# Optimization experiments

Hardware: AMD Instinct MI355X
Metric: run time of the kernel (lower is better)

## Reference

```python
import jax, jax.numpy as jnp
import numpy as np

CLASSES = 21
IOU_THRESH = 0.5
ALPHA = 0.25   # focal loss alpha
GAMMA = 2.0    # focal loss gamma
SL1_BETA = 1.0 # torch SmoothL1Loss default beta
CLS_W = 1.0
REG_W = 1.0
NUM_ANCHORS = 98304
NUM_TARGETS = 1024


def _compute_iou(boxes_a, boxes_b):
    # boxes_a: [T,4], boxes_b: [A,4] in (x1,y1,x2,y2) -> [T,A]
    lt = jnp.maximum(boxes_a[:, None, :2], boxes_b[None, :, :2])
    rb = jnp.minimum(boxes_a[:, None, 2:], boxes_b[None, :, 2:])
    wh = jnp.clip(rb - lt, 0.0)
    inter = wh[..., 0] * wh[..., 1]
    area_a = (boxes_a[:, 2] - boxes_a[:, 0]) * (boxes_a[:, 3] - boxes_a[:, 1])
    area_b = (boxes_b[:, 2] - boxes_b[:, 0]) * (boxes_b[:, 3] - boxes_b[:, 1])
    union = area_a[:, None] + area_b[None, :] - inter
    return inter / jnp.maximum(union, 1e-8)


def _encode(boxes, anchors):
    bw = boxes[:, 2] - boxes[:, 0]
    bh = boxes[:, 3] - boxes[:, 1]
    bcx = boxes[:, 0] + 0.5 * bw
    bcy = boxes[:, 1] + 0.5 * bh
    aw = anchors[:, 2] - anchors[:, 0]
    ah = anchors[:, 3] - anchors[:, 1]
    acx = anchors[:, 0] + 0.5 * aw
    acy = anchors[:, 1] + 0.5 * ah
    tx = (bcx - acx) / aw
    ty = (bcy - acy) / ah
    tw = jnp.log(jnp.maximum(bw, 1e-8) / aw)
    th = jnp.log(jnp.maximum(bh, 1e-8) / ah)
    return jnp.stack([tx, ty, tw, th], axis=1)


def _focal_loss(logits, targets):
    # elementwise sigmoid focal loss (no reduction)
    p = jax.nn.sigmoid(logits)
    # numerically stable BCE with logits
    ce = jnp.maximum(logits, 0.0) - logits * targets + jnp.log1p(jnp.exp(-jnp.abs(logits)))
    p_t = p * targets + (1.0 - p) * (1.0 - targets)
    alpha_t = ALPHA * targets + (1.0 - ALPHA) * (1.0 - targets)
    return alpha_t * (1.0 - p_t) ** GAMMA * ce


def _smooth_l1(diff):
    ad = jnp.abs(diff)
    return jnp.where(ad < SL1_BETA, 0.5 * diff * diff / SL1_BETA, ad - 0.5 * SL1_BETA)


def setup_inputs() -> dict:
    key = jax.random.key(0)
    kA, kW, kT, kJ, kL, kC, kB = jax.random.split(key, 7)
    A, T = NUM_ANCHORS, NUM_TARGETS
    centers = jax.random.uniform(kA, (A, 2), minval=0.15, maxval=0.85)
    sizes = jax.random.uniform(kW, (A, 2), minval=0.05, maxval=0.30)
    anchors = jnp.concatenate([centers - 0.5 * sizes, centers + 0.5 * sizes], axis=1)
    # targets = jittered anchors so IoU >= 0.5 matches exist
    idx = jax.random.randint(kT, (T,), 0, A)
    jitter = jax.random.uniform(kJ, (T, 4), minval=-0.01, maxval=0.01)
    target_boxes = anchors[idx] + jitter
    target_labels = jax.random.randint(kL, (T,), 0, CLASSES)
    classification_preds = jax.random.normal(kC, (A, CLASSES), dtype=jnp.float32)
    boxes_preds = jax.random.normal(kB, (A, 4), dtype=jnp.float32)
    return {
        'classification_preds': classification_preds,
        'boxes_preds': boxes_preds,
        'anchors': anchors,
        'target_boxes': target_boxes,
        'target_labels': target_labels,
    }


def reference(classification_preds, boxes_preds, anchors, target_boxes, target_labels):
    iou = _compute_iou(target_boxes, anchors)  # [T, A]

    # anchor-side matching -> classification targets
    max_iou_for_anchors = jnp.max(iou, axis=0)          # [A]
    target_ids_for_anchors = jnp.argmax(iou, axis=0)     # [A]
    positive_mask = max_iou_for_anchors >= IOU_THRESH    # [A] bool
    n_pos = jnp.sum(positive_mask.astype(jnp.float32))
    onehot = jax.nn.one_hot(target_labels[target_ids_for_anchors], CLASSES, dtype=jnp.float32)
    cls_targets = jnp.where(positive_mask[:, None], onehot, 0.0)
    cls_loss = jnp.sum(_focal_loss(classification_preds, cls_targets)) / n_pos

    max_iou_for_targets = jnp.max(iou, axis=1)          # [T]
    anchor_ids_for_targets = jnp.argmax(iou, axis=1)     # [T]
    t_mask = (max_iou_for_targets >= IOU_THRESH).astype(jnp.float32)  # [T]
    matched_anchors = anchors[anchor_ids_for_targets]    # [T,4]
    encoded = _encode(target_boxes, matched_anchors)     # [T,4]
    pred = boxes_preds[anchor_ids_for_targets]           # [T,4]
    diff = (pred - encoded) * t_mask[:, None]
    n_match = jnp.maximum(jnp.sum(t_mask), 1.0)
    reg_loss = jnp.sum(_smooth_l1(diff)) / (n_match * 4.0)  # mean over matched elements

    w_cls = cls_loss * CLS_W
    w_reg = reg_loss * REG_W
    return (w_cls + w_reg, w_cls, w_reg)
```

## Files before the change

kernel.cpp:

```cpp
#include <hip/hip_runtime.h>
#include <stdint.h>

#define NA 98304
#define NT 1024
#define NC 21
#define NBLK 1536
#define HI_MIN 0xBF000000u
#define C3S 0.33333f

typedef unsigned int u32;
typedef unsigned long long u64;


__device__ __forceinline__ float f0(float x) {
    const float ax = fabsf(x);
    const float u  = __expf(-ax);
    const float ce = fmaxf(x, 0.f) + __logf(1.f + u);
    const float p  = (x >= 0.f ? 1.f : u) / (1.f + u);
    return 0.75f * p * p * ce;
}
__device__ __forceinline__ float f1(float x) {
    const float ax = fabsf(x);
    const float u  = __expf(-ax);
    const float ce = fmaxf(x, 0.f) - x + __logf(1.f + u);
    const float p  = (x >= 0.f ? 1.f : u) / (1.f + u);
    const float q  = 1.f - p;
    return 0.25f * q * q * ce;
}
__device__ __forceinline__ u64 mk_key(float iou, u32 idx) {
    return ((u64)(__float_as_uint(iou) | 0x80000000u) << 32) |
           (u64)(0xFFFFFFFFu - idx);
}
__device__ __forceinline__ float smooth_l1(float d) {
    const float ad = fabsf(d);
    return (ad < 1.f) ? 0.5f * d * d : ad - 0.5f;
}
__device__ __forceinline__ u64 aload64(const u64* p) {
    return __hip_atomic_load(p, __ATOMIC_RELAXED, __HIP_MEMORY_SCOPE_AGENT);
}
__device__ __forceinline__ float aloadf(const float* p) {
    return __hip_atomic_load(p, __ATOMIC_RELAXED, __HIP_MEMORY_SCOPE_AGENT);
}
__device__ __forceinline__ int aloadi(const int* p) {
    return __hip_atomic_load(p, __ATOMIC_RELAXED, __HIP_MEMORY_SCOPE_AGENT);
}

#define CHECK(k, tkk)                                                       \
    {                                                                       \
        const float w0 = fminf(ac.z, tz[k]) + fminf(ac.x, ntx[k]);          \
        const float w  = fmaxf(w0, 0.f);                                    \
        const float h0 = fminf(ac.w, tw4[k]) + fminf(ac.y, nty[k]);         \
        if (fmaf(w, h0, narc) >= sac[k]) {                                  \
            const float h     = fmaxf(h0, 0.f);                             \
            const float inter = w * h;                                      \
            const float arj   = (ac.z + ac.x) * (ac.w + ac.y);              \
            const float sa    = (tz[k] + ntx[k]) * (tw4[k] + nty[k]);       \
            const float uni   = (arj + sa) - inter;                         \
            const float iou   = inter / uni;                                \
            const u64 nk = mk_key(iou, (u32)(b * 64 + j));                  \
            if (nk > tkk) tkk = nk;                                         \
            atomicMax(&s_ak[j], mk_key(iou, (u32)(t0 + 64 * k)));           \
        }                                                                   \
    }

__global__ __launch_bounds__(256) void k_all(
    const float* __restrict__ preds,
    const float4* __restrict__ preds4,
    const int* __restrict__ tlabels,
    const float4* __restrict__ anchors,
    const float4* __restrict__ tboxes,
    const float4* __restrict__ bpreds,
    u64* __restrict__ tkeys,
    float* __restrict__ part,
    int* __restrict__ npos_part,
    int* __restrict__ done_g,
    int* __restrict__ done2,
    float* __restrict__ out)
{
    __shared__ float4 s_anc[64];
    __shared__ float  s_narc[64];
    __shared__ u64    s_ak[64];
    __shared__ float  s_f[4];
    __shared__ int    s_fin;
    __shared__ double s_d[4];
    __shared__ int    s_i[4];
    __shared__ float  s_s[4], s_m[4];

    const int tid  = threadIdx.x;
    const int b    = blockIdx.x;
    const int lane = tid & 63, wid = tid >> 6;

    if (tid < 64) {
        const float4 A = anchors[b * 64 + tid];
        s_anc[tid]  = make_float4(-A.x, -A.y, A.z, A.w);
        s_narc[tid] = -(((A.z - A.x) * (A.w - A.y)) * C3S);
        s_ak[tid]   = 0ull;
    }

    const int t0 = wid * 256 + lane;
    float tz[4], ntx[4], tw4[4], nty[4], sac[4];
    #pragma unroll
    for (int k = 0; k < 4; ++k) {
        const float4 tb = tboxes[t0 + 64 * k];
        tz[k]  = tb.z;  ntx[k] = -tb.x;
        tw4[k] = tb.w;  nty[k] = -tb.y;
        sac[k] = ((tb.z - tb.x) * (tb.w - tb.y)) * C3S;
    }

    float facc;
    {
        const int pb = b * 336;
        const float4 v0 = preds4[pb + tid];
        facc = (f0(v0.x) + f0(v0.y)) + (f0(v0.z) + f0(v0.w));
        if (tid < 80) {
            const float4 v1 = preds4[pb + 256 + tid];
            facc += (f0(v1.x) + f0(v1.y)) + (f0(v1.z) + f0(v1.w));
        }
    }

    u64 tk0 = 0ull, tk1 = 0ull, tk2 = 0ull, tk3 = 0ull;
    __syncthreads();

    #pragma unroll 8
    for (int j = 0; j < 64; ++j) {
        const float4 ac  = s_anc[j];
        const float narc = s_narc[j];
        CHECK(0, tk0)
        CHECK(1, tk1)
        CHECK(2, tk2)
        CHECK(3, tk3)
    }

    for (int o = 32; o > 0; o >>= 1) facc += __shfl_down(facc, o);
    if (lane == 0) s_f[wid] = facc;

    if (tk0 != 0ull) atomicMax(&tkeys[t0],       tk0);
    if (tk1 != 0ull) atomicMax(&tkeys[t0 +  64], tk1);
    if (tk2 != 0ull) atomicMax(&tkeys[t0 + 128], tk2);
    if (tk3 != 0ull) atomicMax(&tkeys[t0 + 192], tk3);

    __syncthreads();

    float corrv = 0.f;
    int   cnt   = 0;
    if (tid < 64) {
        const u64 k0 = s_ak[tid];
        if ((u32)(k0 >> 32) >= HI_MIN) {
            cnt = 1;
            const int tI  = (int)(0xFFFFFFFFu - (u32)k0);
            const int lab = tlabels[tI];
            const float x = preds[(b * 64 + tid) * NC + lab];
            corrv = f1(x) - f0(x);
        }
        for (int o = 32; o > 0; o >>= 1) {
            corrv += __shfl_down(corrv, o);
            cnt   += __shfl_down(cnt, o);
        }
    }
    if (tid == 0) {
        __hip_atomic_store(&part[b], (s_f[0] + s_f[1] + s_f[2] + s_f[3]) + corrv,
                           __ATOMIC_RELAXED, __HIP_MEMORY_SCOPE_AGENT);
        __hip_atomic_store(&npos_part[b], cnt,
                           __ATOMIC_RELAXED, __HIP_MEMORY_SCOPE_AGENT);
    }
    __syncthreads();
    if (tid == 0) {
        __threadfence();
        int fin = 0;
        if (atomicAdd(&done_g[b & 63], 1) == 23) {
            __threadfence();
            fin = (atomicAdd(done2, 1) == 63);
        }
        s_fin = fin;
    }
    __syncthreads();
    if (!s_fin) return;
    __builtin_amdgcn_fence(__ATOMIC_ACQUIRE, "agent");

    double cl = 0.0;
    int    np = 0;
    #pragma unroll
    for (int j = 0; j < 6; ++j) {
        const int i = tid + 256 * j;
        cl += (double)aloadf(&part[i]);
        np += aloadi(&npos_part[i]);
    }
    float s = 0.f, m = 0.f;
    #pragma unroll
    for (int j = 0; j < 4; ++j) {
        const int t = tid + 256 * j;
        const u64 key = aload64(&tkeys[t]);
        if ((u32)(key >> 32) >= HI_MIN) {
            const u32 ga = 0xFFFFFFFFu - (u32)key;
            const float4 tb  = tboxes[t];
            const float4 abx = anchors[ga];
            const float4 pb  = bpreds[ga];
            const float bw = tb.z - tb.x, bh = tb.w - tb.y;
            const float bcx = tb.x + 0.5f * bw, bcy = tb.y + 0.5f * bh;
            const float aw = abx.z - abx.x, ah = abx.w - abx.y;
            const float acx = abx.x + 0.5f * aw, acy = abx.y + 0.5f * ah;
            const float tx = (bcx - acx) / aw;
            const float ty = (bcy - acy) / ah;
            const float tw = logf(fmaxf(bw, 1e-8f) / aw);
            const float th = logf(fmaxf(bh, 1e-8f) / ah);
            s += smooth_l1(pb.x - tx) + smooth_l1(pb.y - ty) +
                 smooth_l1(pb.z - tw) + smooth_l1(pb.w - th);
            m += 1.f;
        }
    }
    for (int o = 32; o > 0; o >>= 1) {
        cl += __shfl_down(cl, o);
        np += __shfl_down(np, o);
        s  += __shfl_down(s, o);
        m  += __shfl_down(m, o);
    }
    __syncthreads();
    if (lane == 0) { s_d[wid] = cl; s_i[wid] = np; s_s[wid] = s; s_m[wid] = m; }
    __syncthreads();
    if (tid == 0) {
        const double cls_sum = s_d[0] + s_d[1] + s_d[2] + s_d[3];
        const int    npos    = s_i[0] + s_i[1] + s_i[2] + s_i[3];
        const float  rs      = s_s[0] + s_s[1] + s_s[2] + s_s[3];
        const float  rm      = s_m[0] + s_m[1] + s_m[2] + s_m[3];
        const float cls = (float)(cls_sum / (double)npos);
        const float reg = rs / (fmaxf(rm, 1.f) * 4.f);
        out[0] = cls + reg;
        out[1] = cls;
        out[2] = reg;
    }
}

extern "C" void kernel_launch(void* const* d_in, const int* in_sizes, int n_in,
                              void* d_out, int out_size, void* d_ws, size_t ws_size,
                              hipStream_t stream) {
    const float*  preds   = (const float*)d_in[0];
    const float4* preds4  = (const float4*)d_in[0];
    const float4* bpreds  = (const float4*)d_in[1];
    const float4* anchors = (const float4*)d_in[2];
    const float4* tboxes  = (const float4*)d_in[3];
    const int*    tlabels = (const int*)d_in[4];

    char* ws = (char*)d_ws;
    int*  done2     = (int*)(ws + 0);
    int*  done_g    = (int*)(ws + 128);
    float* part     = (float*)(ws + 1024);
    int*  npos_part = (int*)(ws + 8192);
    u64*  tkeys     = (u64*)(ws + 16384);

    hipMemsetAsync(d_ws, 0, 1024, stream);

    k_all<<<dim3(NBLK), 256, 0, stream>>>(
        preds, preds4, tlabels, anchors, tboxes, bpreds,
        tkeys, part, npos_part, done_g, done2, (float*)d_out);
}
```

Measured before the change: 127.5 us.

## Bucket anchors spatially and cull targets per bucket before IoU matching

Adds a scatter kernel that bins anchors into 4096 buckets by center position and size, then each main block processes one bucket and keeps only the targets whose centers fall near the bucket's bounding range, so IoU is evaluated on far fewer anchor-target pairs than the dense 64x1024 tile. Overflowing anchors go to a spill list that the final block handles serially. The cost is an extra kernel launch, global atomics for bucketing, and a larger memset. The spill path is sequential with block-wide syncs per anchor and could be slow if many anchors spill.

New measurement: 192.2 us. 1.51x slower.

```diff
diff --git a/kernel.cpp b/kernel.cpp
--- a/kernel.cpp
+++ b/kernel.cpp
@@ -4,7 +4,9 @@
 #define NA 98304
 #define NT 1024
 #define NC 21
-#define NBLK 1536
+#define NBUCK 4096
+#define CAP 64
+#define GRID_MAIN 4096
 #define HI_MIN 0xBF000000u
 #define C3S 0.33333f
 
@@ -44,44 +46,93 @@
 __device__ __forceinline__ int aloadi(const int* p) {
     return __hip_atomic_load(p, __ATOMIC_RELAXED, __HIP_MEMORY_SCOPE_AGENT);
 }
-
-#define CHECK(k, tkk)                                                       \
+__device__ __forceinline__ int iclamp(int v, int lo, int hi) {
+    return v < lo ? lo : (v > hi ? hi : v);
+}
+
+__global__ __launch_bounds__(256) void k_scatter(
+    const float4* __restrict__ anchors,
+    float4* __restrict__ sortedA, u32* __restrict__ sortedId,
+    int* __restrict__ cursor, int* __restrict__ spillcnt,
+    float4* __restrict__ spillA, u32* __restrict__ spillId)
+{
+    const int a = blockIdx.x * 256 + threadIdx.x;
+    const float4 A = anchors[a];
+    const float acx = (A.x + A.z) * 0.5f, acy = (A.y + A.w) * 0.5f;
+    const float aw  = A.z - A.x,          ah  = A.w - A.y;
+    const int cx = iclamp((int)((acx - 0.15f) * 22.857143f), 0, 15);
+    const int cy = iclamp((int)((acy - 0.15f) * 22.857143f), 0, 15);
+    const int wc = iclamp((int)((aw - 0.05f) * 16.f), 0, 3);
+    const int hc = iclamp((int)((ah - 0.05f) * 16.f), 0, 3);
+    const int bkt = cx + (cy << 4) + ((wc + (hc << 2)) << 8);
+    const int pos = atomicAdd(&cursor[bkt], 1);
+    if (pos < CAP) {
+        sortedA[bkt * CAP + pos]  = A;
+        sortedId[bkt * CAP + pos] = (u32)a;
+    } else {
+        const int sp = atomicAdd(spillcnt, 1);
+        spillA[sp]  = A;
+        spillId[sp] = (u32)a;
+    }
+}
+
+#define SECTION(KKBASE)                                                     \
     {                                                                       \
-        const float w0 = fminf(ac.z, tz[k]) + fminf(ac.x, ntx[k]);          \
-        const float w  = fmaxf(w0, 0.f);                                    \
-        const float h0 = fminf(ac.w, tw4[k]) + fminf(ac.y, nty[k]);         \
-        if (fmaf(w, h0, narc) >= sac[k]) {                                  \
-            const float h     = fmaxf(h0, 0.f);                             \
-            const float inter = w * h;                                      \
-            const float arj   = (ac.z + ac.x) * (ac.w + ac.y);              \
-            const float sa    = (tz[k] + ntx[k]) * (tw4[k] + nty[k]);       \
-            const float uni   = (arj + sa) - inter;                         \
-            const float iou   = inter / uni;                                \
-            const u64 nk = mk_key(iou, (u32)(b * 64 + j));                  \
-            if (nk > tkk) tkk = nk;                                         \
-            atomicMax(&s_ak[j], mk_key(iou, (u32)(t0 + 64 * k)));           \
+        const int s  = tid + (KKBASE);                                      \
+        const bool vs = s < nf;                                             \
+        const float4 tb = vs ? s_ft[s] : make_float4(-1e30f,-1e30f,-1e30f,-1e30f); \
+        const float sacv = vs ? s_fs[s] : 1e30f;                            \
+        const int   fid  = vs ? s_fid[s] : 0;                               \
+        u64 tk = 0ull;                                                      \
+        _Pragma("unroll 2")                                                 \
+        for (int j = 0; j < cnt; ++j) {                                     \
+            const float4 ac  = s_anc[j];                                    \
+            const float narc = s_narc[j];                                   \
+            const float w0 = fminf(ac.z, tb.z) + fminf(ac.x, tb.x);         \
+            const float w  = fmaxf(w0, 0.f);                                \
+            const float h0 = fminf(ac.w, tb.w) + fminf(ac.y, tb.y);         \
+            if (fmaf(w, h0, narc) >= sacv) {                                \
+                const float h     = fmaxf(h0, 0.f);                         \
+                const float inter = w * h;                                  \
+                const float arj   = (ac.z + ac.x) * (ac.w + ac.y);          \
+                const float sa    = (tb.z + tb.x) * (tb.w + tb.y);          \
+                const float uni   = (arj + sa) - inter;                     \
+                const float iou   = inter / uni;                            \
+                const u64 nk = mk_key(iou, s_aid[j]);                       \
+                if (nk > tk) tk = nk;                                       \
+                atomicMax(&s_ak[j], mk_key(iou, (u32)fid));                 \
+            }                                                               \
         }                                                                   \
-    }
-
-__global__ __launch_bounds__(256) void k_all(
+        if (tk != 0ull) atomicMax(&tkeys[fid], tk);                         \
+    }
+
+__global__ __launch_bounds__(256) void k_main(
     const float* __restrict__ preds,
     const float4* __restrict__ preds4,
     const int* __restrict__ tlabels,
     const float4* __restrict__ anchors,
     const float4* __restrict__ tboxes,
     const float4* __restrict__ bpreds,
+    const float4* __restrict__ sortedA, const u32* __restrict__ sortedId,
+    const int* __restrict__ cursor, const int* __restrict__ spillcnt,
+    const float4* __restrict__ spillA, const u32* __restrict__ spillId,
     u64* __restrict__ tkeys,
-    float* __restrict__ part,
-    int* __restrict__ npos_part,
-    int* __restrict__ done_g,
-    int* __restrict__ done2,
+    float* __restrict__ part, int* __restrict__ npos_part,
+    int* __restrict__ done_g, int* __restrict__ done2,
     float* __restrict__ out)
 {
-    __shared__ float4 s_anc[64];
-    __shared__ float  s_narc[64];
-    __shared__ u64    s_ak[64];
+    __shared__ float4 s_anc[CAP];
+    __shared__ float  s_narc[CAP];
+    __shared__ u32    s_aid[CAP];
+    __shared__ u64    s_ak[CAP];
+    __shared__ float4 s_ft[NT];
+    __shared__ float  s_fs[NT];
+    __shared__ int    s_fid[NT];
+    __shared__ int    s_nf;
+    __shared__ float  s_bb[6];
     __shared__ float  s_f[4];
     __shared__ int    s_fin;
+    __shared__ u64    s_sp[4];
     __shared__ double s_d[4];
     __shared__ int    s_i[4];
     __shared__ float  s_s[4], s_m[4];
@@ -89,26 +140,11 @@
     const int tid  = threadIdx.x;
     const int b    = blockIdx.x;
     const int lane = tid & 63, wid = tid >> 6;
-
-    if (tid < 64) {
-        const float4 A = anchors[b * 64 + tid];
-        s_anc[tid]  = make_float4(-A.x, -A.y, A.z, A.w);
-        s_narc[tid] = -(((A.z - A.x) * (A.w - A.y)) * C3S);
-        s_ak[tid]   = 0ull;
-    }
-
-    const int t0 = wid * 256 + lane;
-    float tz[4], ntx[4], tw4[4], nty[4], sac[4];
-    #pragma unroll
-    for (int k = 0; k < 4; ++k) {
-        const float4 tb = tboxes[t0 + 64 * k];
-        tz[k]  = tb.z;  ntx[k] = -tb.x;
-        tw4[k] = tb.w;  nty[k] = -tb.y;
-        sac[k] = ((tb.z - tb.x) * (tb.w - tb.y)) * C3S;
-    }
-
-    float facc;
-    {
+    const int cnt0 = cursor[b];
+    const int cnt  = cnt0 > CAP ? CAP : cnt0;
+
+    float facc = 0.f;
+    if (b < 1536) {
         const int pb = b * 336;
         const float4 v0 = preds4[pb + tid];
         facc = (f0(v0.x) + f0(v0.y)) + (f0(v0.z) + f0(v0.w));
@@ -118,56 +154,96 @@
         }
     }
 
-    u64 tk0 = 0ull, tk1 = 0ull, tk2 = 0ull, tk3 = 0ull;
-    __syncthreads();
-
-    #pragma unroll 8
-    for (int j = 0; j < 64; ++j) {
-        const float4 ac  = s_anc[j];
-        const float narc = s_narc[j];
-        CHECK(0, tk0)
-        CHECK(1, tk1)
-        CHECK(2, tk2)
-        CHECK(3, tk3)
+    if (tid < CAP) {
+        const bool v = tid < cnt;
+        float4 A = make_float4(1e30f, 1e30f, -1e30f, -1e30f);
+        u32 id = 0u;
+        if (v) { A = sortedA[b * CAP + tid]; id = sortedId[b * CAP + tid]; }
+        s_anc[tid]  = make_float4(-A.x, -A.y, A.z, A.w);
+        s_narc[tid] = v ? -(((A.z - A.x) * (A.w - A.y)) * C3S) : -1e30f;
+        s_aid[tid]  = id;
+        s_ak[tid]   = 0ull;
+        const float cx = (A.x + A.z) * 0.5f, cy = (A.y + A.w) * 0.5f;
+        float c1 = v ? cx : 1e30f,  c2 = v ? cx : -1e30f;
+        float c3 = v ? cy : 1e30f,  c4 = v ? cy : -1e30f;
+        float c5 = v ? (A.z - A.x) : 0.f, c6 = v ? (A.w - A.y) : 0.f;
+        for (int o = 32; o > 0; o >>= 1) {
+            c1 = fminf(c1, __shfl_xor(c1, o));
+            c2 = fmaxf(c2, __shfl_xor(c2, o));
+            c3 = fminf(c3, __shfl_xor(c3, o));
+            c4 = fmaxf(c4, __shfl_xor(c4, o));
+            c5 = fmaxf(c5, __shfl_xor(c5, o));
+            c6 = fmaxf(c6, __shfl_xor(c6, o));
+        }
+        if (tid == 0) {
+            s_bb[0] = c1; s_bb[1] = c2; s_bb[2] = c3;
+            s_bb[3] = c4; s_bb[4] = c5; s_bb[5] = c6;
+            s_nf = 0;
+        }
+    }
+    __syncthreads();
+
+    if (cnt > 0) {
+        const float bxl = s_bb[0], bxh = s_bb[1], byl = s_bb[2], byh = s_bb[3];
+        const float awm = s_bb[4], ahm = s_bb[5];
+        #pragma unroll
+        for (int k = 0; k < 4; ++k) {
+            const int t = tid + 256 * k;
+            const float4 tb = tboxes[t];
+            const float tcx = (tb.x + tb.z) * 0.5f, tcy = (tb.y + tb.w) * 0.5f;
+            const float tw = tb.z - tb.x, th = tb.w - tb.y;
+            const float rx = (awm + tw) * 0.5f - fmaxf(awm, tw) * (1.f/3.f) + 1e-3f;
+            const float ry = (ahm + th) * 0.5f - fmaxf(ahm, th) * (1.f/3.f) + 1e-3f;
+            if (tcx >= bxl - rx && tcx <= bxh + rx &&
+                tcy >= byl - ry && tcy <= byh + ry) {
+                const int p = atomicAdd(&s_nf, 1);
+                s_ft[p]  = make_float4(-tb.x, -tb.y, tb.z, tb.w);
+                s_fs[p]  = ((tb.z - tb.x) * (tb.w - tb.y)) * C3S;
+                s_fid[p] = t;
+            }
+        }
+    }
+    __syncthreads();
+    const int nf = s_nf;
+
+    if (cnt > 0 && nf > 0) {
+        SECTION(0)
+        if (nf > 256) SECTION(256)
+        if (nf > 512) SECTION(512)
+        if (nf > 768) SECTION(768)
     }
 
     for (int o = 32; o > 0; o >>= 1) facc += __shfl_down(facc, o);
     if (lane == 0) s_f[wid] = facc;
-
-    if (tk0 != 0ull) atomicMax(&tkeys[t0],       tk0);
-    if (tk1 != 0ull) atomicMax(&tkeys[t0 +  64], tk1);
-    if (tk2 != 0ull) atomicMax(&tkeys[t0 + 128], tk2);
-    if (tk3 != 0ull) atomicMax(&tkeys[t0 + 192], tk3);
-
     __syncthreads();
 
     float corrv = 0.f;
-    int   cnt   = 0;
-    if (tid < 64) {
+    int   cnt2  = 0;
+    if (tid < CAP) {
         const u64 k0 = s_ak[tid];
         if ((u32)(k0 >> 32) >= HI_MIN) {
-            cnt = 1;
+            cnt2 = 1;
             const int tI  = (int)(0xFFFFFFFFu - (u32)k0);
             const int lab = tlabels[tI];
-            const float x = preds[(b * 64 + tid) * NC + lab];
+            const float x = preds[s_aid[tid] * NC + lab];
             corrv = f1(x) - f0(x);
         }
         for (int o = 32; o > 0; o >>= 1) {
             corrv += __shfl_down(corrv, o);
-            cnt   += __shfl_down(cnt, o);
+            cnt2  += __shfl_down(cnt2, o);
         }
     }
     if (tid == 0) {
         __hip_atomic_store(&part[b], (s_f[0] + s_f[1] + s_f[2] + s_f[3]) + corrv,
                            __ATOMIC_RELAXED, __HIP_MEMORY_SCOPE_AGENT);
-        __hip_atomic_store(&npos_part[b], cnt,
+        __hip_atomic_store(&npos_part[b], cnt2,
                            __ATOMIC_RELAXED, __HIP_MEMORY_SCOPE_AGENT);
     }
     __syncthreads();
     if (tid == 0) {
         __threadfence();
         int fin = 0;
-        if (atomicAdd(&done_g[b & 63], 1) == 23) {
+        if (atomicAdd(&done_g[b & 63], 1) == 63) {
             __threadfence();
             fin = (atomicAdd(done2, 1) == 63);
         }
@@ -180,11 +256,57 @@
     double cl = 0.0;
     int    np = 0;
     #pragma unroll
-    for (int j = 0; j < 6; ++j) {
+    for (int j = 0; j < 16; ++j) {
         const int i = tid + 256 * j;
         cl += (double)aloadf(&part[i]);
         np += aloadi(&npos_part[i]);
     }
+
+    const int sc0 = aloadi(spillcnt);
+    const int sc  = sc0 > NA ? NA : sc0;
+    for (int a = 0; a < sc; ++a) {
+        const float4 A = spillA[a];
+        const u32 aid  = spillId[a];
+        const float ar = (A.z - A.x) * (A.w - A.y);
+        u64 bk = 0ull;
+        #pragma unroll
+        for (int k = 0; k < 4; ++k) {
+            const int t = tid + 256 * k;
+            const float4 tb = tboxes[t];
+            const float sa = (tb.z - tb.x) * (tb.w - tb.y);
+            const float w = fmaxf(fminf(A.z, tb.z) - fmaxf(A.x, tb.x), 0.f);
+            const float h = fmaxf(fminf(A.w, tb.w) - fmaxf(A.y, tb.y), 0.f);
+            const float inter = w * h;
+            const float uni   = (ar + sa) - inter;
+            const float iou   = inter / uni;
+            if (iou >= 0.5f) {
+                const u64 nk = mk_key(iou, (u32)t);
+                if (nk > bk) bk = nk;
+                atomicMax(&tkeys[t], mk_key(iou, aid));
+            }
+        }
+        for (int o = 32; o > 0; o >>= 1) {
+            const u64 ob = __shfl_down(bk, o);
+            if (ob > bk) bk = ob;
+        }
+        if (lane == 0) s_sp[wid] = bk;
+        __syncthreads();
+        if (tid == 0) {
+            u64 k0 = s_sp[0];
+            if (s_sp[1] > k0) k0 = s_sp[1];
+            if (s_sp[2] > k0) k0 = s_sp[2];
+            if (s_sp[3] > k0) k0 = s_sp[3];
+            if ((u32)(k0 >> 32) >= HI_MIN) {
+                np += 1;
+                const int tI  = (int)(0xFFFFFFFFu - (u32)k0);
+                const int lab = tlabels[tI];
+                const float x = preds[aid * NC + lab];
+                cl += (double)(f1(x) - f0(x));
+            }
+        }
+        __syncthreads();
+    }
+
     float s = 0.f, m = 0.f;
     #pragma unroll
     for (int j = 0; j < 4; ++j) {
@@ -241,15 +363,25 @@
     const int*    tlabels = (const int*)d_in[4];
 
     char* ws = (char*)d_ws;
-    int*  done2     = (int*)(ws + 0);
-    int*  done_g    = (int*)(ws + 128);
-    float* part     = (float*)(ws + 1024);
-    int*  npos_part = (int*)(ws + 8192);
-    u64*  tkeys     = (u64*)(ws + 16384);
-
-    hipMemsetAsync(d_ws, 0, 1024, stream);
-
-    k_all<<<dim3(NBLK), 256, 0, stream>>>(
+    int*    done2     = (int*)(ws + 0);
+    int*    spillcnt  = (int*)(ws + 4);
+    int*    done_g    = (int*)(ws + 128);
+    int*    cursor    = (int*)(ws + 1024);
+    float*  part      = (float*)(ws + 20480);
+    int*    npos_part = (int*)(ws + 36864);
+    u64*    tkeys     = (u64*)(ws + 53248);
+    float4* sortedA   = (float4*)(ws + 65536);
+    u32*    sortedId  = (u32*)(ws + 4259840);
+    float4* spillA    = (float4*)(ws + 5308416);
+    u32*    spillId   = (u32*)(ws + 6881280);
+
+    hipMemsetAsync(d_ws, 0, 17408, stream);
+
+    k_scatter<<<dim3(384), 256, 0, stream>>>(
+        anchors, sortedA, sortedId, cursor, spillcnt, spillA, spillId);
+
+    k_main<<<dim3(GRID_MAIN), 256, 0, stream>>>(
         preds, preds4, tlabels, anchors, tboxes, bpreds,
+        sortedA, sortedId, cursor, spillcnt, spillA, spillId,
         tkeys, part, npos_part, done_g, done2, (float*)d_out);
 }
```
